# Performance work log

Hardware: AMD Instinct MI355X
Metric: run time of the kernel (lower is better)

The kernel has to match this reference:

```python
import jax, jax.numpy as jnp
import numpy as np

EMBED_DIM = 1024
N_HEADS = 16
HEAD_DIM = EMBED_DIM // N_HEADS


def setup_inputs() -> dict:
    key = jax.random.key(0)
    ks = jax.random.split(key, 9)
    s = 1.0 / np.sqrt(EMBED_DIM)
    x = jax.random.normal(ks[0], (4, 2048, EMBED_DIM), dtype=jnp.float32)
    Wq = jax.random.uniform(ks[1], (EMBED_DIM, EMBED_DIM), jnp.float32, -s, s)
    bq = jax.random.uniform(ks[2], (EMBED_DIM,), jnp.float32, -s, s)
    Wk = jax.random.uniform(ks[3], (EMBED_DIM, EMBED_DIM), jnp.float32, -s, s)
    bk = jax.random.uniform(ks[4], (EMBED_DIM,), jnp.float32, -s, s)
    Wv = jax.random.uniform(ks[5], (EMBED_DIM, EMBED_DIM), jnp.float32, -s, s)
    bv = jax.random.uniform(ks[6], (EMBED_DIM,), jnp.float32, -s, s)
    Wo = jax.random.uniform(ks[7], (EMBED_DIM, EMBED_DIM), jnp.float32, -s, s)
    bo = jax.random.uniform(ks[8], (EMBED_DIM,), jnp.float32, -s, s)
    return {"x": x, "Wq": Wq, "bq": bq, "Wk": Wk, "bk": bk,
            "Wv": Wv, "bv": bv, "Wo": Wo, "bo": bo}


def reference(x, Wq, bq, Wk, bk, Wv, bv, Wo, bo):
    B, S, _ = x.shape
    # projections (PyTorch Linear: x @ W.T + b; weights stored as [in,out] here)
    q = x @ Wq + bq
    k = x @ Wk + bk
    v = x @ Wv + bv
    # [B, H, S, D]
    q = q.reshape(B, S, N_HEADS, HEAD_DIM).transpose(0, 2, 1, 3)
    k = k.reshape(B, S, N_HEADS, HEAD_DIM).transpose(0, 2, 1, 3)
    v = v.reshape(B, S, N_HEADS, HEAD_DIM).transpose(0, 2, 1, 3)
    scores = jnp.einsum('bhsd,bhtd->bhst', q, k) / np.sqrt(HEAD_DIM).astype(np.float32)
    attn = jax.nn.softmax(scores, axis=-1)
    out = jnp.einsum('bhst,bhtd->bhsd', attn, v)
    out = out.transpose(0, 2, 1, 3).reshape(B, S, EMBED_DIM)
    return out @ Wo + bo  # dropout=0 (eval) -> identity
```

## Files before the change

kernel.cpp:

```cpp
#include <hip/hip_runtime.h>
#include <stdint.h>

#define EMBED 1024
#define NH 16
#define HD 64
#define SEQ 2048
#define BATCH 4
#define M_TOT (BATCH*SEQ)
#define QSCALE 0.18033688011112042f

typedef __attribute__((ext_vector_type(8))) short short8;
typedef __attribute__((ext_vector_type(4))) float floatx4;
typedef __attribute__((ext_vector_type(4))) unsigned int uintx4;

__device__ __forceinline__ unsigned short f2bf(float f) {
    union { float f; unsigned int u; } v; v.f = f;
    unsigned int r = v.u + 0x7fffu + ((v.u >> 16) & 1u);
    return (unsigned short)(r >> 16);
}

__device__ __forceinline__ void load_lds16(const unsigned short* g, unsigned short* l) {
    __builtin_amdgcn_global_load_lds(
        (const __attribute__((address_space(1))) unsigned int*)g,
        (__attribute__((address_space(3))) unsigned int*)l, 16, 0, 0);
}

__global__ void cvt_x(const float* __restrict__ x, unsigned short* __restrict__ xb) {
    int i = (blockIdx.x * 256 + threadIdx.x) * 4;
    float4 v = *(const float4*)(x + i);
    ushort4 o;
    o.x = f2bf(v.x); o.y = f2bf(v.y); o.z = f2bf(v.z); o.w = f2bf(v.w);
    *(ushort4*)(xb + i) = o;
}

__global__ void wtrans(const float* __restrict__ w0, const float* __restrict__ w1,
                       const float* __restrict__ w2, const float* __restrict__ w3,
                       unsigned short* __restrict__ t0, unsigned short* __restrict__ t1,
                       unsigned short* __restrict__ t2, unsigned short* __restrict__ t3) {
    __shared__ float tile[32][33];
    const float* W; unsigned short* T;
    switch (blockIdx.z) { case 0: W=w0; T=t0; break; case 1: W=w1; T=t1; break;
                          case 2: W=w2; T=t2; break; default: W=w3; T=t3; }
    int n0 = blockIdx.x * 32, k0 = blockIdx.y * 32;
    int tx = threadIdx.x, ty = threadIdx.y;
    #pragma unroll
    for (int i = 0; i < 4; i++)
        tile[ty + i*8][tx] = W[(k0 + ty + i*8) * EMBED + n0 + tx];
    __syncthreads();
    #pragma unroll
    for (int i = 0; i < 4; i++)
        T[(n0 + ty + i*8) * EMBED + k0 + tx] = f2bf(tile[tx][ty + i*8]);
}

#define GBUFS 8192

template<bool STG, int WAITN>
__device__ __forceinline__ void ktile(int t,
        const unsigned short* Abase, const unsigned short* Bbase,
        const unsigned short* Asrc, const unsigned short* Bsrc,
        unsigned short* sda, unsigned short* sdb, floatx4 (&acc)[4][2]) {
    const int bo = (t & 3) * GBUFS;
    short8 fA[4], fB[2];
    #pragma unroll
    for (int m=0;m<4;m++) fA[m] = *(const short8*)(Abase + bo + m*512);
    #pragma unroll
    for (int n=0;n<2;n++) fB[n] = *(const short8*)(Bbase + bo + n*512);
    if (STG) {
        const int buf_ = (t+3) & 3; const int ko_ = (t+3)*32;
        load_lds16(Asrc + ko_, sda + buf_*GBUFS);
        load_lds16(Bsrc + ko_, sdb + buf_*GBUFS);
    }
    #pragma unroll
    for (int m=0;m<4;m++)
      #pragma unroll
      for (int n=0;n<2;n++)
        acc[m][n] = __builtin_amdgcn_mfma_f32_16x16x32_bf16(fA[m], fB[n], acc[m][n], 0,0,0);
    if (WAITN == 4)      { asm volatile("s_waitcnt vmcnt(4)" ::: "memory"); asm volatile("s_barrier" ::: "memory"); }
    else if (WAITN == 2) { asm volatile("s_waitcnt vmcnt(2)" ::: "memory"); asm volatile("s_barrier" ::: "memory"); }
    else if (WAITN == 0) { asm volatile("s_waitcnt vmcnt(0)" ::: "memory"); asm volatile("s_barrier" ::: "memory"); }
}

template<int MODE>
__global__ __launch_bounds__(512, 4) void gemmk(
        const unsigned short* __restrict__ A, const unsigned short* __restrict__ BT,
        const float* __restrict__ b0, const float* __restrict__ b1, const float* __restrict__ b2,
        void* __restrict__ o0, void* __restrict__ o1, void* __restrict__ o2) {
    constexpr int BM = 128, BN = 128;
    __shared__ unsigned short lds[4*GBUFS];
    const int tid = threadIdx.x;
    const int lane = tid & 63, wave = tid >> 6;
    const int quad = lane >> 4, l16 = lane & 15;
    const int wm = wave >> 2, wn = wave & 3;
    const int id = blockIdx.x;
    constexpr int MS = (M_TOT/BM)/8;
    const int xcd = id & 7, j = id >> 3;
    const int mblk = (xcd * MS + (j % MS)) * BM;
    const int nblk = (j / MS) * BN;

    const int srow = tid >> 2;
    const int scol = ((tid & 3) ^ (srow & 3) ^ ((srow >> 2) & 3)) * 8;
    const unsigned short* Asrc = A  + (size_t)(mblk + srow) * EMBED + scol;
    const unsigned short* Bsrc = BT + (size_t)(nblk + srow) * EMBED + scol;
    unsigned short* sda = lds + wave * 512;
    unsigned short* sdb = lds + BM*32 + wave * 512;

    const int cs = (quad ^ (l16 & 3) ^ ((l16 >> 2) & 3)) * 8;
    const unsigned short* Abase = lds + (wm*64 + l16)*32 + cs;
    const unsigned short* Bbase = lds + BM*32 + (wn*32 + l16)*32 + cs;

    floatx4 acc[4][2];
    #pragma unroll
    for (int m=0;m<4;m++)
      #pragma unroll
      for (int n=0;n<2;n++) acc[m][n] = (floatx4){0.f,0.f,0.f,0.f};

    #pragma unroll
    for (int p=0;p<3;p++) {
        load_lds16(Asrc + p*32, sda + p*GBUFS);
        load_lds16(Bsrc + p*32, sdb + p*GBUFS);
    }
    asm volatile("s_waitcnt vmcnt(4)" ::: "memory");
    asm volatile("s_barrier" ::: "memory");

    #pragma unroll 4
    for (int t = 0; t < 28; ++t)
        ktile<true,4>(t, Abase, Bbase, Asrc, Bsrc, sda, sdb, acc);
    ktile<true, 4>(28, Abase, Bbase, Asrc, Bsrc, sda, sdb, acc);
    ktile<false,2>(29, Abase, Bbase, Asrc, Bsrc, sda, sdb, acc);
    ktile<false,0>(30, Abase, Bbase, Asrc, Bsrc, sda, sdb, acc);
    ktile<false,-1>(31, Abase, Bbase, Asrc, Bsrc, sda, sdb, acc);

    if constexpr (MODE == 1) {
        float* O = (float*)o0;
        #pragma unroll
        for (int mt=0;mt<4;mt++)
          #pragma unroll
          for (int nt=0;nt<2;nt++) {
            int col = nblk + wn*32 + nt*16 + l16;
            float bv = b0[col];
            #pragma unroll
            for (int r=0;r<4;r++) {
                int row = mblk + wm*64 + mt*16 + quad*4 + r;
                O[(size_t)row * EMBED + col] = acc[mt][nt][r] + bv;
            }
          }
    } else {
        int which = nblk >> 10;
        const float* bs = (which==0) ? b0 : (which==1) ? b1 : b2;
        if (which < 2) {
            unsigned short* O = (unsigned short*)((which==0) ? o0 : o1);
            float sc = (which==0) ? QSCALE : 1.f;
            #pragma unroll
            for (int mt=0;mt<4;mt++)
              #pragma unroll
              for (int nt=0;nt<2;nt++) {
                int coll = (nblk & 1023) + wn*32 + nt*16 + l16;
                float bv = bs[coll];
                int h = coll >> 6, d = coll & 63;
                #pragma unroll
                for (int r=0;r<4;r++) {
                    int row = mblk + wm*64 + mt*16 + quad*4 + r;
                    int b = row >> 11, s = row & 2047;
                    O[((size_t)(b*NH + h)*SEQ + s)*HD + d] = f2bf((acc[mt][nt][r] + bv) * sc);
                }
              }
        } else {
            unsigned short* T = lds;
            unsigned short* OV = (unsigned short*)o2;
            size_t rowbase = ((size_t)((mblk >> 11)*1024 + (nblk & 1023))) * SEQ + (mblk & 2047);
            __syncthreads();
            #pragma unroll
            for (int nt=0;nt<2;nt++) {
                int cloc = wn*32 + nt*16 + l16;
                float bv = bs[(nblk & 1023) + cloc];
                #pragma unroll
                for (int mt=0;mt<4;mt++) {
                    int row0 = wm*64 + mt*16 + quad*4;
                    int sp0 = (row0 & ~31) | (((row0 >> 2) & 3) << 3) | (((row0 >> 4) & 1) << 2);
                    ushort4 w;
                    w.x = f2bf(acc[mt][nt][0] + bv);
                    w.y = f2bf(acc[mt][nt][1] + bv);
                    w.z = f2bf(acc[mt][nt][2] + bv);
                    w.w = f2bf(acc[mt][nt][3] + bv);
                    *(ushort4*)(T + cloc*136 + sp0) = w;
                }
            }
            __syncthreads();
            int s0 = (lane & 15) * 8, dloc = lane >> 4;
            #pragma unroll
            for (int i=0;i<4;i++) {
                int c = wave*16 + i*4 + dloc;
                short8 v = *(const short8*)(T + c*136 + s0);
                *(short8*)(OV + rowbase + (size_t)c * SEQ + s0) = v;
            }
        }
    }
}

__global__ __launch_bounds__(512, 4) void attn(
    const unsigned short* __restrict__ Q, const unsigned short* __restrict__ K,
    const unsigned short* __restrict__ VTp, unsigned short* __restrict__ O) {
    __shared__ unsigned short kv[2][4096];
    unsigned short* kvf = &kv[0][0];
    int tid = threadIdx.x;
    int lane = tid & 63, wave = tid >> 6;
    int quad = lane >> 4, l16 = lane & 15;
    int id = blockIdx.x;
    int bh = (id & 7) * 8 + (id >> 6);
    int qblk = (id >> 3) & 7;
    int b = bh >> 4, h = bh & 15;
    int q0 = qblk * 256 + wave * 32;
    const unsigned short* Qb = Q + (size_t)bh * SEQ * HD;
    const unsigned short* Kb = K + (size_t)bh * SEQ * HD;
    const unsigned short* Vb = VTp + (size_t)bh * HD * SEQ;
    int li = (wave & 3) * 64 + lane;
    const unsigned short* src;
    int dstofs = (wave & 3) * 512 + ((wave >> 2) ? 2048 : 0);
    int src_step;
    if (wave < 4) {
        int t = li >> 3, slot = li & 7;
        int dblk = slot ^ (t & 7);
        src = Kb + (size_t)t * HD + dblk * 8;
        src_step = 32 * HD;
    } else {
        int d = li >> 2, slot = li & 3;
        int swz = (d & 3) ^ ((d >> 2) & 3);
        src = Vb + (size_t)d * SEQ + (slot ^ swz) * 8;
        src_step = 32;
    }
    short8 qf[2][2];
    #pragma unroll
    for (int mt=0;mt<2;mt++) {
        const unsigned short* qp = Qb + (size_t)(q0 + mt*16 + l16) * HD + quad*8;
        qf[mt][0] = *(const short8*)(qp);
        qf[mt][1] = *(const short8*)(qp + 32);
    }
    floatx4 o_acc[2][4], l_acc[2];
    #pragma unroll
    for (int mt=0;mt<2;mt++) {
        l_acc[mt] = (floatx4){0.f,0.f,0.f,0.f};
        #pragma unroll
        for (int dt=0;dt<4;dt++) o_acc[mt][dt] = (floatx4){0.f,0.f,0.f,0.f};
    }
    short8 ones;
    #pragma unroll
    for (int jj=0;jj<8;jj++) ones[jj] = (short)0x3F80;
    int koff[2][2], voff[4];
    #pragma unroll
    for (int nt=0;nt<2;nt++) {
        int t = nt*16 + l16;
        #pragma unroll
        for (int hh=0;hh<2;hh++)
            koff[nt][hh] = t*64 + ((hh*4 + quad) ^ (t & 7)) * 8;
    }
    #pragma unroll
    for (int dt=0;dt<4;dt++) {
        int d = dt*16 + l16;
        voff[dt] = 2048 + d*32 + ((quad ^ (d & 3) ^ ((d >> 2) & 3))) * 8;
    }

    load_lds16(src, kvf + dstofs);
    src += src_step;

    for (int it = 0; it < 64; ++it) {
        const unsigned short* kb = kvf + (it & 1) * 4096;
        if (it < 63) {
            load_lds16(src, kvf + ((it & 1) ^ 1) * 4096 + dstofs);
            src += src_step;
            asm volatile("s_waitcnt vmcnt(1)" ::: "memory");
        } else {
            asm volatile("s_waitcnt vmcnt(0)" ::: "memory");
        }
        __builtin_amdgcn_s_barrier();
        asm volatile("" ::: "memory");
        short8 kf[2][2], vf[4];
        #pragma unroll
        for (int nt=0;nt<2;nt++) {
            kf[nt][0] = *(const short8*)(kb + koff[nt][0]);
            kf[nt][1] = *(const short8*)(kb + koff[nt][1]);
        }
        #pragma unroll
        for (int dt=0;dt<4;dt++)
            vf[dt] = *(const short8*)(kb + voff[dt]);
        floatx4 sacc[2][2];
        __builtin_amdgcn_s_setprio(1);
        #pragma unroll
        for (int nt=0;nt<2;nt++)
          #pragma unroll
          for (int mt=0;mt<2;mt++) {
            floatx4 s = (floatx4){0.f,0.f,0.f,0.f};
            s = __builtin_amdgcn_mfma_f32_16x16x32_bf16(kf[nt][0], qf[mt][0], s, 0, 0, 0);
            s = __builtin_amdgcn_mfma_f32_16x16x32_bf16(kf[nt][1], qf[mt][1], s, 0, 0, 0);
            sacc[nt][mt] = s;
          }
        __builtin_amdgcn_s_setprio(0);
        short8 pf[2];
        #pragma unroll
        for (int mt=0;mt<2;mt++) {
            uintx4 pu;
            #pragma unroll
            for (int jp=0;jp<4;jp++) {
                int nt = jp >> 1, rp = (jp & 1) * 2;
                float e0 = __builtin_amdgcn_exp2f(sacc[nt][mt][rp]);
                float e1 = __builtin_amdgcn_exp2f(sacc[nt][mt][rp+1]);
                unsigned int w;
                asm("v_cvt_pk_bf16_f32 %0, %1, %2" : "=v"(w) : "v"(e0), "v"(e1));
                pu[jp] = w;
            }
            pf[mt] = __builtin_bit_cast(short8, pu);
        }
        __builtin_amdgcn_s_setprio(1);
        #pragma unroll
        for (int mt=0;mt<2;mt++) {
            l_acc[mt] = __builtin_amdgcn_mfma_f32_16x16x32_bf16(ones, pf[mt], l_acc[mt], 0, 0, 0);
            #pragma unroll
            for (int dt=0;dt<4;dt++)
                o_acc[mt][dt] = __builtin_amdgcn_mfma_f32_16x16x32_bf16(vf[dt], pf[mt], o_acc[mt][dt], 0, 0, 0);
        }
        __builtin_amdgcn_s_setprio(0);
        asm volatile("" ::: "memory");
        __builtin_amdgcn_s_barrier();
    }
    #pragma unroll
    for (int mt=0;mt<2;mt++) {
        float inv = 1.f / l_acc[mt][0];
        int s = q0 + mt*16 + l16;
        #pragma unroll
        for (int dt=0;dt<4;dt++) {
            ushort4 w;
            w.x = f2bf(o_acc[mt][dt][0]*inv);
            w.y = f2bf(o_acc[mt][dt][1]*inv);
            w.z = f2bf(o_acc[mt][dt][2]*inv);
            w.w = f2bf(o_acc[mt][dt][3]*inv);
            *(ushort4*)(O + ((size_t)b*SEQ + s)*EMBED + h*HD + dt*16 + quad*4) = w;
        }
    }
}

extern "C" void kernel_launch(void* const* d_in, const int* in_sizes, int n_in,
                              void* d_out, int out_size, void* d_ws, size_t ws_size,
                              hipStream_t stream) {
    const float* x  = (const float*)d_in[0];
    const float* Wq = (const float*)d_in[1]; const float* bq = (const float*)d_in[2];
    const float* Wk = (const float*)d_in[3]; const float* bk = (const float*)d_in[4];
    const float* Wv = (const float*)d_in[5]; const float* bv = (const float*)d_in[6];
    const float* Wo = (const float*)d_in[7]; const float* bo = (const float*)d_in[8];
    char* ws = (char*)d_ws;
    unsigned short* xb  = (unsigned short*)(ws);
    unsigned short* WqT = (unsigned short*)(ws + (16ull<<20));
    unsigned short* WkT = (unsigned short*)(ws + (18ull<<20));
    unsigned short* WvT = (unsigned short*)(ws + (20ull<<20));
    unsigned short* WoT = (unsigned short*)(ws + (22ull<<20));
    unsigned short* Qb  = (unsigned short*)(ws + (24ull<<20));
    unsigned short* Kb  = (unsigned short*)(ws + (40ull<<20));
    unsigned short* VTb = (unsigned short*)(ws + (56ull<<20));
    unsigned short* Ob  = xb;

    cvt_x<<<(M_TOT*EMBED)/1024, 256, 0, stream>>>(x, xb);
    wtrans<<<dim3(32,32,4), dim3(32,8), 0, stream>>>(Wq,Wk,Wv,Wo, WqT,WkT,WvT,WoT);
    gemmk<0><<<dim3(1536), 512, 0, stream>>>(xb, WqT, bq, bk, bv, Qb, Kb, VTb);
    attn<<<dim3(512), 512, 0, stream>>>(Qb, Kb, VTb, Ob);
    gemmk<1><<<dim3(512), 512, 0, stream>>>(Ob, WoT, bo, bo, bo, (float*)d_out, nullptr, nullptr);
}
```

Before: 248.6 us.

## Double KV tile to 64 keys per iteration in attention loop

The attention kernel now processes 64 keys per iteration instead of 32. The LDS tiles are doubled, so the loop runs 32 times instead of 64, which halves the barriers and the waits on global loads per key. K and V fragments are now read from LDS just before each MFMA rather than all up front, with a new swizzle for the wider V rows. The cost is twice the LDS per block and more live accumulator registers, which may limit occupancy at 4 blocks per CU.

New measurement: 260.2 us. 1.05x slower.

```diff
diff --git a/kernel.cpp b/kernel.cpp
--- a/kernel.cpp
+++ b/kernel.cpp
@@ -200,7 +200,7 @@
 __global__ __launch_bounds__(512, 4) void attn(
     const unsigned short* __restrict__ Q, const unsigned short* __restrict__ K,
     const unsigned short* __restrict__ VTp, unsigned short* __restrict__ O) {
-    __shared__ unsigned short kv[2][4096];
+    __shared__ unsigned short kv[2][8192];
     unsigned short* kvf = &kv[0][0];
     int tid = threadIdx.x;
     int lane = tid & 63, wave = tid >> 6;
@@ -213,20 +213,24 @@
     const unsigned short* Qb = Q + (size_t)bh * SEQ * HD;
     const unsigned short* Kb = K + (size_t)bh * SEQ * HD;
     const unsigned short* Vb = VTp + (size_t)bh * HD * SEQ;
-    int li = (wave & 3) * 64 + lane;
-    const unsigned short* src;
-    int dstofs = (wave & 3) * 512 + ((wave >> 2) ? 2048 : 0);
-    int src_step;
-    if (wave < 4) {
-        int t = li >> 3, slot = li & 7;
-        int dblk = slot ^ (t & 7);
-        src = Kb + (size_t)t * HD + dblk * 8;
-        src_step = 32 * HD;
-    } else {
-        int d = li >> 2, slot = li & 3;
-        int swz = (d & 3) ^ ((d >> 2) & 3);
-        src = Vb + (size_t)d * SEQ + (slot ^ swz) * 8;
-        src_step = 32;
+    int wk = wave & 3, lrow = lane >> 3, lslot = lane & 7;
+    const unsigned short *src0, *src1;
+    int dst0, dst1, src_step;
+    {
+        int c0 = wk*2, c1 = wk*2 + 1;
+        int r0 = c0*8 + lrow, r1 = c1*8 + lrow;
+        int sc = (lslot ^ lrow) * 8;
+        if (wave < 4) {
+            src0 = Kb + (size_t)r0 * HD + sc;
+            src1 = Kb + (size_t)r1 * HD + sc;
+            dst0 = c0*512; dst1 = c1*512;
+            src_step = 64 * HD;
+        } else {
+            src0 = Vb + (size_t)r0 * SEQ + sc;
+            src1 = Vb + (size_t)r1 * SEQ + sc;
+            dst0 = 4096 + c0*512; dst1 = 4096 + c1*512;
+            src_step = 64;
+        }
     }
     short8 qf[2][2];
     #pragma unroll
@@ -245,9 +249,9 @@
     short8 ones;
     #pragma unroll
     for (int jj=0;jj<8;jj++) ones[jj] = (short)0x3F80;
-    int koff[2][2], voff[4];
-    #pragma unroll
-    for (int nt=0;nt<2;nt++) {
+    int koff[4][2], voff[4][2];
+    #pragma unroll
+    for (int nt=0;nt<4;nt++) {
         int t = nt*16 + l16;
         #pragma unroll
         for (int hh=0;hh<2;hh++)
@@ -256,67 +260,75 @@
     #pragma unroll
     for (int dt=0;dt<4;dt++) {
         int d = dt*16 + l16;
-        voff[dt] = 2048 + d*32 + ((quad ^ (d & 3) ^ ((d >> 2) & 3))) * 8;
-    }
-
-    load_lds16(src, kvf + dstofs);
-    src += src_step;
-
-    for (int it = 0; it < 64; ++it) {
-        const unsigned short* kb = kvf + (it & 1) * 4096;
-        if (it < 63) {
-            load_lds16(src, kvf + ((it & 1) ^ 1) * 4096 + dstofs);
-            src += src_step;
-            asm volatile("s_waitcnt vmcnt(1)" ::: "memory");
+        #pragma unroll
+        for (int g=0;g<2;g++)
+            voff[dt][g] = 4096 + d*64 + ((g*4 + quad) ^ (d & 7)) * 8;
+    }
+
+    load_lds16(src0, kvf + dst0);
+    load_lds16(src1, kvf + dst1);
+    src0 += src_step; src1 += src_step;
+
+    for (int it = 0; it < 32; ++it) {
+        const unsigned short* kb = kvf + (it & 1) * 8192;
+        if (it < 31) {
+            int bo = ((it & 1) ^ 1) * 8192;
+            load_lds16(src0, kvf + bo + dst0);
+            load_lds16(src1, kvf + bo + dst1);
+            src0 += src_step; src1 += src_step;
+            asm volatile("s_waitcnt vmcnt(2)" ::: "memory");
         } else {
             asm volatile("s_waitcnt vmcnt(0)" ::: "memory");
         }
         __builtin_amdgcn_s_barrier();
         asm volatile("" ::: "memory");
-        short8 kf[2][2], vf[4];
-        #pragma unroll
-        for (int nt=0;nt<2;nt++) {
-            kf[nt][0] = *(const short8*)(kb + koff[nt][0]);
-            kf[nt][1] = *(const short8*)(kb + koff[nt][1]);
-        }
-        #pragma unroll
-        for (int dt=0;dt<4;dt++)
-            vf[dt] = *(const short8*)(kb + voff[dt]);
-        floatx4 sacc[2][2];
+        floatx4 sacc[4][2];
         __builtin_amdgcn_s_setprio(1);
         #pragma unroll
-        for (int nt=0;nt<2;nt++)
+        for (int nt=0;nt<4;nt++) {
+            short8 kf0 = *(const short8*)(kb + koff[nt][0]);
+            short8 kf1 = *(const short8*)(kb + koff[nt][1]);
+            #pragma unroll
+            for (int mt=0;mt<2;mt++) {
+                floatx4 s = (floatx4){0.f,0.f,0.f,0.f};
+                s = __builtin_amdgcn_mfma_f32_16x16x32_bf16(kf0, qf[mt][0], s, 0, 0, 0);
+                s = __builtin_amdgcn_mfma_f32_16x16x32_bf16(kf1, qf[mt][1], s, 0, 0, 0);
+                sacc[nt][mt] = s;
+            }
+        }
+        __builtin_amdgcn_s_setprio(0);
+        short8 pf[2][2];
+        #pragma unroll
+        for (int mt=0;mt<2;mt++)
           #pragma unroll
-          for (int mt=0;mt<2;mt++) {
-            floatx4 s = (floatx4){0.f,0.f,0.f,0.f};
-            s = __builtin_amdgcn_mfma_f32_16x16x32_bf16(kf[nt][0], qf[mt][0], s, 0, 0, 0);
-            s = __builtin_amdgcn_mfma_f32_16x16x32_bf16(kf[nt][1], qf[mt][1], s, 0, 0, 0);
-            sacc[nt][mt] = s;
-          }
-        __builtin_amdgcn_s_setprio(0);
-        short8 pf[2];
-        #pragma unroll
-        for (int mt=0;mt<2;mt++) {
+          for (int g=0;g<2;g++) {
             uintx4 pu;
             #pragma unroll
             for (int jp=0;jp<4;jp++) {
-                int nt = jp >> 1, rp = (jp & 1) * 2;
+                int nt = g*2 + (jp >> 1), rp = (jp & 1) * 2;
                 float e0 = __builtin_amdgcn_exp2f(sacc[nt][mt][rp]);
                 float e1 = __builtin_amdgcn_exp2f(sacc[nt][mt][rp+1]);
                 unsigned int w;
                 asm("v_cvt_pk_bf16_f32 %0, %1, %2" : "=v"(w) : "v"(e0), "v"(e1));
                 pu[jp] = w;
             }
-            pf[mt] = __builtin_bit_cast(short8, pu);
-        }
+            pf[mt][g] = __builtin_bit_cast(short8, pu);
+          }
         __builtin_amdgcn_s_setprio(1);
         #pragma unroll
         for (int mt=0;mt<2;mt++) {
-            l_acc[mt] = __builtin_amdgcn_mfma_f32_16x16x32_bf16(ones, pf[mt], l_acc[mt], 0, 0, 0);
-            #pragma unroll
-            for (int dt=0;dt<4;dt++)
-                o_acc[mt][dt] = __builtin_amdgcn_mfma_f32_16x16x32_bf16(vf[dt], pf[mt], o_acc[mt][dt], 0, 0, 0);
-        }
+            l_acc[mt] = __builtin_amdgcn_mfma_f32_16x16x32_bf16(ones, pf[mt][0], l_acc[mt], 0, 0, 0);
+            l_acc[mt] = __builtin_amdgcn_mfma_f32_16x16x32_bf16(ones, pf[mt][1], l_acc[mt], 0, 0, 0);
+        }
+        #pragma unroll
+        for (int dt=0;dt<4;dt++)
+          #pragma unroll
+          for (int g=0;g<2;g++) {
+            short8 vf = *(const short8*)(kb + voff[dt][g]);
+            #pragma unroll
+            for (int mt=0;mt<2;mt++)
+                o_acc[mt][dt] = __builtin_amdgcn_mfma_f32_16x16x32_bf16(vf, pf[mt][g], o_acc[mt][dt], 0, 0, 0);
+          }
         __builtin_amdgcn_s_setprio(0);
         asm volatile("" ::: "memory");
         __builtin_amdgcn_s_barrier();
```
